# Kernel optimization log

Hardware: AMD Instinct MI355X
Metric: run time of the kernel (lower is better)

The kernel has to match this reference:

```python
import jax, jax.numpy as jnp
import numpy as np

DEPTH = 6
D_IN = 512
D_OUT = 256
NUM_NODES = 2 ** (DEPTH + 1) - 1   # 127
NUM_LEAVES = 2 ** (DEPTH + 1)      # 128
BATCH = 8192
EPS = 0.01


def _routes(depth):
    num_nodes = 2 ** (depth + 1) - 1
    num_leaves = 2 ** (depth + 1)
    idxs = np.zeros((num_leaves, depth + 1), np.int32)
    sides = np.zeros((num_leaves, depth + 1), np.int32)
    for i in range(num_leaves):
        temp, temp_sides = [], []
        leaf_idx = num_nodes + i
        for _ in range(depth):
            parent_idx = (leaf_idx - 1) // 2
            temp.append(parent_idx)
            temp_sides.append(1 if (leaf_idx - 1) % 2 == 0 else 0)
            leaf_idx = parent_idx
        temp_sides.append(1 if (leaf_idx - 1) % 2 == 0 else 0)
        temp.append(0)
        idxs[i] = temp[::-1]
        sides[i] = temp_sides[::-1]
    return idxs, sides


def _l2norm(v, axis):
    # matches torch F.normalize (eps=1e-12)
    n = jnp.sqrt(jnp.sum(v * v, axis=axis, keepdims=True))
    return v / jnp.maximum(n, 1e-12)


def setup_inputs() -> dict:
    key = jax.random.key(0)
    ks = jax.random.split(key, 6)
    D1 = D_IN + 1  # pre-network output dim
    x = jax.random.normal(ks[0], (BATCH, D_IN), jnp.float32)
    # pre_network Linear(D_IN, D_IN+1)
    W_pre = jax.random.normal(ks[1], (D1, D_IN), jnp.float32) * (1.0 / np.sqrt(D_IN))
    b_pre = jax.random.normal(ks[2], (D1,), jnp.float32) * 0.01
    # node hyperplanes [num_nodes, D1]
    right_w = jax.random.normal(ks[3], (NUM_NODES, D1), jnp.float32)
    # leaves Linear(D1, out*num_leaves)
    W_leaf = jax.random.normal(ks[4], (D_OUT * NUM_LEAVES, D1), jnp.float32) * (1.0 / np.sqrt(D1))
    b_leaf = jax.random.normal(ks[5], (D_OUT * NUM_LEAVES,), jnp.float32) * 0.01
    idxs, sides = _routes(DEPTH)
    return {
        "x": x, "W_pre": W_pre, "b_pre": b_pre, "right_w": right_w,
        "W_leaf": W_leaf, "b_leaf": b_leaf,
        "route_idx": jnp.asarray(idxs, jnp.int32),
        "route_side": jnp.asarray(sides, jnp.int32),
    }


def reference(x, W_pre, b_pre, right_w, W_leaf, b_leaf, route_idx, route_side):
    b = x.shape[0]
    # pre-network: Linear + ReLU  -> [b, D1]
    h = jax.nn.relu(x @ W_pre.T + b_pre)
    # node probabilities (cosine-similarity routing)
    nx = _l2norm(h, axis=1)                  # [b, D1]
    nw = _l2norm(right_w, axis=1)            # [N, D1]
    right = nx @ nw.T                        # [b, N]
    right_dist = (1.0 - right) / 2.0
    left_dist = 1.0 - right_dist
    # all_indices [2, N, b]
    all_ind = jnp.stack([right_dist.T, left_dist.T], axis=0)
    # gather route probs -> [L, depth+1, b]
    probs = all_ind[route_side, route_idx]
    log_probs = jnp.log(jnp.clip(probs, EPS, 1.0 - EPS))
    leaves_logp = jnp.sum(log_probs, axis=1)        # [L, b]
    s_w = jnp.exp(leaves_logp)                       # [L, b]
    entropy = -jnp.sum(s_w * leaves_logp, axis=0)    # [b]
    max_entropy = (NUM_LEAVES / DEPTH) * jnp.log(jnp.float32(DEPTH))
    entropy_loss = entropy / max_entropy
    # all leaf outputs at once -> [b, L, out]
    results = (h @ W_leaf.T + b_leaf).reshape(b, NUM_LEAVES, D_OUT)
    # NOTE: original multiplies by (randn(1) + 1 + entropy_loss.mean());
    # the randn(1) term is fixed to 0 for a deterministic reference.
    scale = 1.0 + jnp.mean(entropy_loss)
    out = jnp.sum(results * scale * s_w.T[:, :, None], axis=1)  # [b, out]
    return out
```

## Files before the change

### kernel.cpp

```cpp
#include <hip/hip_runtime.h>

typedef _Float16 f16;
typedef unsigned short u16;
typedef unsigned int u32;
typedef _Float16 f16x8 __attribute__((ext_vector_type(8)));
typedef float f32x4 __attribute__((ext_vector_type(4)));
typedef float f32x16 __attribute__((ext_vector_type(16)));

union F16x8U { f16x8 v; uint4 q; u16 us[8]; f16 h[8]; };
union HBits { f16 f; u16 u; };

#define GLD16(g, l)                                                        \
  __builtin_amdgcn_global_load_lds(                                        \
      (const __attribute__((address_space(1))) void*)(g),                  \
      (__attribute__((address_space(3))) void*)(l), 16, 0, 0)

__global__ void kcvt_all(const float* __restrict__ x, f16* __restrict__ xo,
                         const float* __restrict__ w, f16* __restrict__ wo,
                         const float* __restrict__ rwsrc, f16* __restrict__ ro,
                         const float* __restrict__ wl, const float* __restrict__ blf,
                         f16* __restrict__ wpk) {
  int b = blockIdx.x;
  if (b < 2048) {
    int i = (b * 256 + threadIdx.x) << 3;
    float4 a = *(const float4*)(x + i);
    float4 c = *(const float4*)(x + i + 4);
    F16x8U u;
    u.h[0] = (f16)a.x; u.h[1] = (f16)a.y; u.h[2] = (f16)a.z; u.h[3] = (f16)a.w;
    u.h[4] = (f16)c.x; u.h[5] = (f16)c.y; u.h[6] = (f16)c.z; u.h[7] = (f16)c.w;
    *(uint4*)(xo + i) = u.q;
  } else if (b < 2336) {
    int e = ((b - 2048) * 256 + threadIdx.x) << 2;
    int row = e >> 9, col = e & 511;
    union { uint2 q; f16 h[4]; } u;
    if (row < 513) {
      float4 v = *(const float4*)(w + (size_t)row * 512 + col);
      u.h[0] = (f16)v.x; u.h[1] = (f16)v.y; u.h[2] = (f16)v.z; u.h[3] = (f16)v.w;
    } else {
      u.h[0] = u.h[1] = u.h[2] = u.h[3] = (f16)0.0f;
    }
    *(uint2*)(wo + e) = u.q;
  } else if (b < 2408) {
    int e = ((b - 2336) * 256 + threadIdx.x) << 2;
    int row = e / 576, c0 = e - row * 576;
    union { uint2 q; f16 h[4]; } u;
#pragma unroll
    for (int i = 0; i < 4; ++i) {
      int c = c0 + i;
      float v = (row < 127 && c < 513) ? rwsrc[(size_t)row * 513 + c] : 0.0f;
      u.h[i] = (f16)v;
    }
    *(uint2*)(ro + e) = u.q;
  } else {
    int e = ((b - 2408) * 256 + threadIdx.x) << 3;
    int row = e / 544, c0 = e - row * 544;
    const float* src = wl + (size_t)row * 513 + c0;
    F16x8U u;
#pragma unroll
    for (int i = 0; i < 8; ++i) {
      int c = c0 + i;
      float v = (c < 513) ? src[i] : ((c == 513) ? blf[row] : 0.0f);
      u.h[i] = (f16)v;
    }
    *(uint4*)(wpk + e) = u.q;
  }
}

template <int MODE>
__global__ __launch_bounds__(256, 2) void kgemm(
    const f16* __restrict__ A, const f16* __restrict__ B,
    const float* __restrict__ bias, void* __restrict__ C,
    int NK, int astr, int bstr) {
  __shared__ alignas(16) f16 al[2][128 * 32];
  __shared__ alignas(16) f16 bl[2][64 * 40];
  const int tid = threadIdx.x, lane = tid & 63, wid = tid >> 6;
  const int wm = wid >> 1, wn = wid & 1;
  const int brow = blockIdx.x << 7, bcol = blockIdx.y << 6;

  int arow[2], aseg[2];
#pragma unroll
  for (int i = 0; i < 2; ++i) { int c = i * 256 + tid; arow[i] = c >> 2; aseg[i] = c & 3; }
  int br0 = tid / 5, bs0 = tid - br0 * 5;
  int c1 = 256 + lane;
  int br1 = c1 / 5, bs1 = c1 - br1 * 5;

  f32x4 acc[4][2];
#pragma unroll
  for (int mf = 0; mf < 4; ++mf)
#pragma unroll
    for (int nf = 0; nf < 2; ++nf)
#pragma unroll
      for (int j = 0; j < 4; ++j) acc[mf][nf][j] = 0.0f;

  auto stage = [&](int kc, int bf) {
    int kcol = kc << 5;
#pragma unroll
    for (int i = 0; i < 2; ++i) {
      f16* ldsb = &al[bf][(i * 256 + (wid << 6)) << 3];
      GLD16(A + (size_t)(brow + arow[i]) * astr + kcol + (aseg[i] << 3), ldsb);
    }
    {
      f16* ldsb = &bl[bf][(wid << 6) << 3];
      GLD16(B + (size_t)(bcol + br0) * bstr + kcol + (bs0 < 4 ? (bs0 << 3) : 0), ldsb);
    }
    if (wid == 0) {
      f16* ldsb = &bl[bf][256 << 3];
      GLD16(B + (size_t)(bcol + br1) * bstr + kcol + (bs1 < 4 ? (bs1 << 3) : 0), ldsb);
    }
  };

  stage(0, 0);
  __syncthreads();
  int cur = 0;
  for (int kc = 0; kc < NK; ++kc) {
    if (kc + 1 < NK) stage(kc + 1, cur ^ 1);
    f16x8 af[4], bfm[2];
#pragma unroll
    for (int mf = 0; mf < 4; ++mf)
      af[mf] = *(const f16x8*)&al[cur][((wm << 6) + (mf << 4) + (lane & 15)) * 32 + ((lane >> 4) << 3)];
#pragma unroll
    for (int nf = 0; nf < 2; ++nf)
      bfm[nf] = *(const f16x8*)&bl[cur][((wn << 5) + (nf << 4) + (lane & 15)) * 40 + ((lane >> 4) << 3)];
#pragma unroll
    for (int mf = 0; mf < 4; ++mf)
#pragma unroll
      for (int nf = 0; nf < 2; ++nf)
        acc[mf][nf] = __builtin_amdgcn_mfma_f32_16x16x32_f16(af[mf], bfm[nf], acc[mf][nf], 0, 0, 0);
    __syncthreads();
    cur ^= 1;
  }

#pragma unroll
  for (int mf = 0; mf < 4; ++mf) {
#pragma unroll
    for (int nf = 0; nf < 2; ++nf) {
      int gcol = bcol + (wn << 5) + (nf << 4) + (lane & 15);
      int gr0 = brow + (wm << 6) + (mf << 4) + ((lane >> 4) << 2);
      if (MODE == 0) {
        float bv = (gcol < 513) ? bias[gcol] : 0.0f;
#pragma unroll
        for (int j = 0; j < 4; ++j) {
          float v = fmaxf(acc[mf][nf][j] + bv, 0.0f);
          ((f16*)C)[(size_t)(gr0 + j) * 576 + gcol] = (gcol == 513) ? (f16)1.0f : (f16)v;
        }
      } else {
#pragma unroll
        for (int j = 0; j < 4; ++j)
          ((float*)C)[(size_t)(gr0 + j) * 128 + gcol] = acc[mf][nf][j];
      }
    }
  }
}

__global__ void khnorm(const f16* __restrict__ hf, float* __restrict__ ihn) {
  int row = (blockIdx.x << 2) + (threadIdx.x >> 6);
  int lane = threadIdx.x & 63;
  float s = 0.0f;
  for (int c = lane; c < 513; c += 64) {
    float v = (float)hf[(size_t)row * 576 + c];
    s += v * v;
  }
  for (int o = 32; o; o >>= 1) s += __shfl_down(s, o);
  if (!lane) ihn[row] = 1.0f / fmaxf(sqrtf(s), 1e-12f);
}

__global__ void kinvrw(const float* __restrict__ rw, float* __restrict__ irw) {
  int j = (blockIdx.x << 2) + (threadIdx.x >> 6);
  if (j >= 127) return;
  int lane = threadIdx.x & 63;
  float s = 0.0f;
  for (int d = lane; d < 513; d += 64) {
    float v = rw[(size_t)j * 513 + d];
    s += v * v;
  }
  for (int o = 32; o; o >>= 1) s += __shfl_down(s, o);
  if (!lane) irw[j] = 1.0f / fmaxf(sqrtf(s), 1e-12f);
}

__global__ void kroute(const float* __restrict__ G, const float* __restrict__ ihn,
                       const float* __restrict__ irw, u16* __restrict__ swh,
                       float* __restrict__ entp) {
  int b = blockIdx.x * 128 + threadIdx.x;
  float ih = ihn[b];
  const float* g = G + (size_t)b * 128;
  float ent = 0.0f;
  size_t wbase = (size_t)(b & ~127) + (((b & 31) >> 1) << 3) + ((b & 1) << 2) + ((b >> 5) & 3);
  float lp[8]; int nd[8];
  nd[0] = 0; lp[0] = 0.0f;
  for (int l = 0; l < 128; ++l) {
    int d0 = l ? (6 - __builtin_ctz(l)) : 0;
#pragma unroll
    for (int d = 0; d < 7; ++d) {
      if (d >= d0) {
        int n = nd[d];
        int bit = (l >> (6 - d)) & 1;
        float cs = g[n] * ih * irw[n];
        float pr = bit ? 0.5f * (1.0f - cs) : 0.5f * (1.0f + cs);
        pr = fminf(fmaxf(pr, 0.01f), 0.99f);
        lp[d + 1] = lp[d] + __logf(pr);
        nd[d + 1] = 2 * n + 1 + bit;
      }
    }
    float sw = __expf(lp[7]);
    ent -= sw * lp[7];
    HBits hb; hb.f = (f16)sw;
    swh[(size_t)l * 8192 + wbase] = hb.u;
  }
  for (int o = 32; o; o >>= 1) ent += __shfl_down(ent, o);
  __shared__ float red[2];
  if (!(threadIdx.x & 63)) red[threadIdx.x >> 6] = ent;
  __syncthreads();
  if (!threadIdx.x) atomicAdd(entp, red[0] + red[1]);
}

__global__ __launch_bounds__(512, 4) void kbig(
    const f16* __restrict__ hf, const f16* __restrict__ wp,
    const u16* __restrict__ swh, const float* __restrict__ entp,
    float* __restrict__ out) {
  __shared__ alignas(16) char smem[73728];

  const int tid = threadIdx.x, lane = tid & 63, wid = tid >> 6;
  const int obl = blockIdx.x & 7, mb = blockIdx.x >> 3;
  const int brow = mb << 7, ocol = obl << 5;

#pragma unroll
  for (int i = 0; i < 4; ++i) {
    int c = i * 512 + tid;
    int l = c >> 4, rg = c & 15;
    GLD16(swh + (size_t)l * 8192 + mb * 128 + rg * 8,
          smem + ((i * 512 + (wid << 6)) << 4));
  }
  auto stageA = [&](int kcp) {
    int c = tid & 255, q = c >> 7, row = c & 127;
    GLD16(hf + (size_t)(brow + row) * 576 + kcp * 16 + q * 8,
          smem + 65536 + ((kcp & 1) << 12) + ((wid & 3) << 10));
  };
  auto stageB = [&](int s2) {
    int kcp = s2 >> 4, lgp = s2 & 15;
    int col = lane & 31, q = (lane >> 5) & 1;
    GLD16(wp + (size_t)((lgp * 8 + wid) * 256 + ocol + col) * 544 + kcp * 16 + q * 8,
          smem + 32768 + ((s2 & 3) << 13) + (wid << 10));
  };
  stageA(0);
  stageB(0);
  stageB(1);

  f32x16 acc[4];
#pragma unroll
  for (int mf = 0; mf < 4; ++mf)
#pragma unroll
    for (int j = 0; j < 16; ++j) acc[mf][j] = 0.0f;

  f16x8 afr[4];
  const int aoff = 65536 + ((lane >> 5) << 11) + ((lane & 31) << 4);
  const int boffc = 32768 + (wid << 10) + ((lane >> 5) << 9) + ((lane & 31) << 4);
  const int swoff = (lane & 31) << 3;

  for (int kc8 = 0; kc8 < 33; ++kc8) {
    const bool tail = (kc8 == 32);
#pragma unroll
    for (int pp = 0; pp < 8; ++pp) {
      const int p = kc8 * 8 + pp;
      const int s0 = 2 * p;
      if (!tail || pp < 7) { stageB(s0 + 2); stageB(s0 + 3); }
      if (pp == 4 && !tail) stageA(kc8 + 1);
      if (tail && pp == 7)         asm volatile("s_waitcnt vmcnt(0)" ::: "memory");
      else if (pp == 4 || pp == 5) asm volatile("s_waitcnt vmcnt(3)" ::: "memory");
      else                         asm volatile("s_waitcnt vmcnt(2)" ::: "memory");
      __builtin_amdgcn_s_barrier();
      __builtin_amdgcn_sched_barrier(0);
      if (pp == 0) {
#pragma unroll
        for (int mf = 0; mf < 4; ++mf)
          afr[mf] = *(const f16x8*)(smem + aoff + ((kc8 & 1) << 12) + (mf << 9));
      }
      const int bufA = (pp & 1) << 1;
      uint2 swqA = *(const uint2*)(smem + ((pp * 16 + wid) << 8) + swoff);
      f16x8 bfA = *(const f16x8*)(smem + boffc + (bufA << 13));
      uint2 swqB = *(const uint2*)(smem + ((pp * 16 + 8 + wid) << 8) + swoff);
      f16x8 bfB = *(const f16x8*)(smem + boffc + ((bufA + 1) << 13));
      __builtin_amdgcn_s_setprio(1);
      {
        const u16* sc = (const u16*)&swqA;
#pragma unroll
        for (int mf = 0; mf < 4; ++mf) {
          HBits hb; hb.u = sc[mf];
          f16x8 as = afr[mf] * hb.f;
          acc[mf] = __builtin_amdgcn_mfma_f32_32x32x16_f16(as, bfA, acc[mf], 0, 0, 0);
        }
      }
      {
        const u16* sc = (const u16*)&swqB;
#pragma unroll
        for (int mf = 0; mf < 4; ++mf) {
          HBits hb; hb.u = sc[mf];
          f16x8 as = afr[mf] * hb.f;
          acc[mf] = __builtin_amdgcn_mfma_f32_32x32x16_f16(as, bfB, acc[mf], 0, 0, 0);
        }
      }
      __builtin_amdgcn_s_setprio(0);
      __builtin_amdgcn_sched_barrier(0);
    }
  }

  __syncthreads();
  auto writeAcc = [&](char* base) {
#pragma unroll
    for (int mf = 0; mf < 4; ++mf)
#pragma unroll
      for (int rq = 0; rq < 4; ++rq)
        *(f32x4*)(base + ((((mf << 2) + rq) << 6) + lane) * 16) =
            ((const f32x4*)&acc[mf])[rq];
  };
  auto addAcc = [&](const char* base) {
#pragma unroll
    for (int mf = 0; mf < 4; ++mf)
#pragma unroll
      for (int rq = 0; rq < 4; ++rq) {
        f32x4 v = *(const f32x4*)(base + ((((mf << 2) + rq) << 6) + lane) * 16);
        ((f32x4*)&acc[mf])[rq] += v;
      }
  };
  if (wid >= 4) writeAcc(smem + ((wid - 4) << 14));
  __syncthreads();
  if (wid < 4) addAcc(smem + (wid << 14));
  __syncthreads();
  if (wid == 2 || wid == 3) writeAcc(smem + ((wid - 2) << 14));
  __syncthreads();
  if (wid < 2) addAcc(smem + (wid << 14));
  __syncthreads();
  if (wid == 1) writeAcc(smem);
  __syncthreads();
  if (wid == 0) {
    addAcc(smem);
    float scale = 1.0f + (*entp) / (8192.0f * (128.0f / 6.0f) * logf(6.0f));
#pragma unroll
    for (int mf = 0; mf < 4; ++mf)
#pragma unroll
      for (int r = 0; r < 16; ++r) {
        int row = brow + (mf << 5) + (r & 3) + ((r >> 2) << 3) + ((lane >> 5) << 2);
        out[(size_t)row * 256 + ocol + (lane & 31)] = scale * acc[mf][r];
      }
  }
}

extern "C" void kernel_launch(void* const* d_in, const int* in_sizes, int n_in,
                              void* d_out, int out_size, void* d_ws, size_t ws_size,
                              hipStream_t stream) {
  const float* x     = (const float*)d_in[0];
  const float* wpre  = (const float*)d_in[1];
  const float* bpre  = (const float*)d_in[2];
  const float* rw    = (const float*)d_in[3];
  const float* wleaf = (const float*)d_in[4];
  const float* bleaf = (const float*)d_in[5];
  float* out = (float*)d_out;

  char* ws = (char*)d_ws;
  constexpr size_t O_ENT = 0;
  constexpr size_t O_XO  = 256;
  constexpr size_t O_WPO = O_XO  + 8388608;
  constexpr size_t O_RWO = O_WPO + 589824;
  constexpr size_t O_IRW = O_RWO + 147456;
  constexpr size_t O_HO  = O_IRW + 512;
  constexpr size_t O_IHN = O_HO  + 9437184;
  constexpr size_t O_G   = O_IHN + 32768;
  constexpr size_t O_SWH = O_G   + 4194304;
  constexpr size_t O_WPK = O_SWH + 2097152;

  float* ent = (float*)(ws + O_ENT);
  f16* xo   = (f16*)(ws + O_XO);
  f16* wpo  = (f16*)(ws + O_WPO);
  f16* rwo  = (f16*)(ws + O_RWO);
  float* irw = (float*)(ws + O_IRW);
  f16* ho   = (f16*)(ws + O_HO);
  float* ihn = (float*)(ws + O_IHN);
  float* go = (float*)(ws + O_G);
  u16* swh  = (u16*)(ws + O_SWH);
  f16* wpk  = (f16*)(ws + O_WPK);

  hipMemsetAsync(ent, 0, sizeof(float), stream);
  kcvt_all<<<11112, 256, 0, stream>>>(x, xo, wpre, wpo, rw, rwo, wleaf, bleaf, wpk);
  kgemm<0><<<dim3(64, 9), 256, 0, stream>>>(xo, wpo, bpre, (void*)ho, 16, 512, 512);
  khnorm<<<2048, 256, 0, stream>>>(ho, ihn);
  kinvrw<<<32, 256, 0, stream>>>(rw, irw);
  kgemm<1><<<dim3(64, 2), 256, 0, stream>>>(ho, rwo, nullptr, (void*)go, 17, 576, 576);
  kroute<<<64, 128, 0, stream>>>(go, ihn, irw, swh, ent);
  kbig<<<512, 512, 0, stream>>>(ho, wpk, swh, ent, out);
}
```

Before: 583.1 us.

## Deepen B-tile ring to five slots and drop per-step barriers in kbig

Replaces the 4-slot double-step B staging with a 5-slot ring that prefetches two steps further ahead. It also removes the per-iteration workgroup barrier, relying on each wave loading its own B slice. The A tile is now staged per-wave with a barrier only at A refills. The next step's B and weight fragments are read from LDS before the current MFMA cluster, to hide LDS latency. This raises LDS use to 80KB, which may hurt occupancy. It risks races if any LDS data is shared across waves without synchronisation.

```diff
diff --git a/kernel.cpp b/kernel.cpp
--- a/kernel.cpp
+++ b/kernel.cpp
@@ -217,33 +217,46 @@
     const f16* __restrict__ hf, const f16* __restrict__ wp,
     const u16* __restrict__ swh, const float* __restrict__ entp,
     float* __restrict__ out) {
-  __shared__ alignas(16) char smem[73728];
+  __shared__ alignas(16) char smem[81920];
 
   const int tid = threadIdx.x, lane = tid & 63, wid = tid >> 6;
   const int obl = blockIdx.x & 7, mb = blockIdx.x >> 3;
   const int brow = mb << 7, ocol = obl << 5;
 
+  auto stageA = [&](int kcp) {
+    const int buf = kcp & 1;
+#pragma unroll
+    for (int seg = 0; seg < 4; ++seg) {
+      int c = seg * 64 + lane, q = c >> 7, row = c & 127;
+      GLD16(hf + (size_t)(brow + row) * 576 + kcp * 16 + q * 8,
+            smem + 73728 + (buf << 12) + (seg << 10));
+    }
+  };
+  auto stageB = [&](int s) {
+    int lgp = s & 15, kcp = s >> 4, slot = s % 5;
+    GLD16(wp + (size_t)((lgp * 8 + wid) * 256 + ocol + (lane & 31)) * 544 +
+              kcp * 16 + ((lane >> 5) & 1) * 8,
+          smem + 32768 + slot * 8192 + (wid << 10));
+  };
+  auto rdSW = [&](int s) -> uint2 {
+    return *(const uint2*)(smem + ((s & 15) * 8 + wid) * 256 + ((lane & 31) << 3));
+  };
+  auto rdB = [&](int s) -> f16x8 {
+    return *(const f16x8*)(smem + 32768 + (s % 5) * 8192 + (wid << 10) +
+                           ((lane >> 5) << 9) + ((lane & 31) << 4));
+  };
+
 #pragma unroll
   for (int i = 0; i < 4; ++i) {
     int c = i * 512 + tid;
-    int l = c >> 4, rg = c & 15;
-    GLD16(swh + (size_t)l * 8192 + mb * 128 + rg * 8,
+    GLD16(swh + (size_t)(c >> 4) * 8192 + mb * 128 + (c & 15) * 8,
           smem + ((i * 512 + (wid << 6)) << 4));
   }
-  auto stageA = [&](int kcp) {
-    int c = tid & 255, q = c >> 7, row = c & 127;
-    GLD16(hf + (size_t)(brow + row) * 576 + kcp * 16 + q * 8,
-          smem + 65536 + ((kcp & 1) << 12) + ((wid & 3) << 10));
-  };
-  auto stageB = [&](int s2) {
-    int kcp = s2 >> 4, lgp = s2 & 15;
-    int col = lane & 31, q = (lane >> 5) & 1;
-    GLD16(wp + (size_t)((lgp * 8 + wid) * 256 + ocol + col) * 544 + kcp * 16 + q * 8,
-          smem + 32768 + ((s2 & 3) << 13) + (wid << 10));
-  };
   stageA(0);
-  stageB(0);
-  stageB(1);
+  stageB(0); stageB(1); stageB(2); stageB(3);
+  asm volatile("s_waitcnt vmcnt(0)" ::: "memory");
+  __builtin_amdgcn_sched_barrier(0);
+  __builtin_amdgcn_s_barrier();
 
   f32x16 acc[4];
 #pragma unroll
@@ -252,54 +265,50 @@
     for (int j = 0; j < 16; ++j) acc[mf][j] = 0.0f;
 
   f16x8 afr[4];
-  const int aoff = 65536 + ((lane >> 5) << 11) + ((lane & 31) << 4);
-  const int boffc = 32768 + (wid << 10) + ((lane >> 5) << 9) + ((lane & 31) << 4);
-  const int swoff = (lane & 31) << 3;
+  uint2 swP = rdSW(0);
+  f16x8 bfP = rdB(0);
+
+  auto cluster = [&](uint2 swq, f16x8 bf) {
+    const u16* sc = (const u16*)&swq;
+    __builtin_amdgcn_s_setprio(1);
+#pragma unroll
+    for (int mf = 0; mf < 4; ++mf) {
+      HBits hb; hb.u = sc[mf];
+      f16x8 as = afr[mf] * hb.f;
+      acc[mf] = __builtin_amdgcn_mfma_f32_32x32x16_f16(as, bf, acc[mf], 0, 0, 0);
+    }
+    __builtin_amdgcn_s_setprio(0);
+  };
 
   for (int kc8 = 0; kc8 < 33; ++kc8) {
-    const bool tail = (kc8 == 32);
 #pragma unroll
     for (int pp = 0; pp < 8; ++pp) {
-      const int p = kc8 * 8 + pp;
-      const int s0 = 2 * p;
-      if (!tail || pp < 7) { stageB(s0 + 2); stageB(s0 + 3); }
-      if (pp == 4 && !tail) stageA(kc8 + 1);
-      if (tail && pp == 7)         asm volatile("s_waitcnt vmcnt(0)" ::: "memory");
-      else if (pp == 4 || pp == 5) asm volatile("s_waitcnt vmcnt(3)" ::: "memory");
-      else                         asm volatile("s_waitcnt vmcnt(2)" ::: "memory");
-      __builtin_amdgcn_s_barrier();
+      const int p = kc8 * 8 + pp, s0 = 2 * p;
+      if (!(kc8 == 32 && pp >= 6)) { stageB(s0 + 4); stageB(s0 + 5); }
+      if (pp == 4 && kc8 < 32) {
+        __builtin_amdgcn_s_barrier();
+        stageA(kc8 + 1);
+      }
+      if (kc8 == 32 && pp == 6)      asm volatile("s_waitcnt vmcnt(1)" ::: "memory");
+      else if (kc8 == 32 && pp == 7) asm volatile("s_waitcnt vmcnt(0)" ::: "memory");
+      else if ((pp == 4 || pp == 5) && kc8 < 32)
+                                     asm volatile("s_waitcnt vmcnt(6)" ::: "memory");
+      else                           asm volatile("s_waitcnt vmcnt(2)" ::: "memory");
       __builtin_amdgcn_sched_barrier(0);
       if (pp == 0) {
 #pragma unroll
         for (int mf = 0; mf < 4; ++mf)
-          afr[mf] = *(const f16x8*)(smem + aoff + ((kc8 & 1) << 12) + (mf << 9));
-      }
-      const int bufA = (pp & 1) << 1;
-      uint2 swqA = *(const uint2*)(smem + ((pp * 16 + wid) << 8) + swoff);
-      f16x8 bfA = *(const f16x8*)(smem + boffc + (bufA << 13));
-      uint2 swqB = *(const uint2*)(smem + ((pp * 16 + 8 + wid) << 8) + swoff);
-      f16x8 bfB = *(const f16x8*)(smem + boffc + ((bufA + 1) << 13));
-      __builtin_amdgcn_s_setprio(1);
-      {
-        const u16* sc = (const u16*)&swqA;
-#pragma unroll
-        for (int mf = 0; mf < 4; ++mf) {
-          HBits hb; hb.u = sc[mf];
-          f16x8 as = afr[mf] * hb.f;
-          acc[mf] = __builtin_amdgcn_mfma_f32_32x32x16_f16(as, bfA, acc[mf], 0, 0, 0);
-        }
-      }
-      {
-        const u16* sc = (const u16*)&swqB;
-#pragma unroll
-        for (int mf = 0; mf < 4; ++mf) {
-          HBits hb; hb.u = sc[mf];
-          f16x8 as = afr[mf] * hb.f;
-          acc[mf] = __builtin_amdgcn_mfma_f32_32x32x16_f16(as, bfB, acc[mf], 0, 0, 0);
-        }
-      }
-      __builtin_amdgcn_s_setprio(0);
-      __builtin_amdgcn_sched_barrier(0);
+          afr[mf] = *(const f16x8*)(smem + 73728 + ((kc8 & 1) << 12) +
+                                    ((lane >> 5) << 11) + (mf << 9) + ((lane & 31) << 4));
+      }
+      uint2 swC = rdSW(s0 + 1);
+      f16x8 bfC = rdB(s0 + 1);
+      cluster(swP, bfP);
+      cluster(swC, bfC);
+      if (p < 263) {
+        swP = rdSW(s0 + 2);
+        bfP = rdB(s0 + 2);
+      }
     }
   }
 
```

After: 618.3 us. 1.06x slower.
